# Performance work log

Measured on AMD Instinct MI355X. Metric: run time of the kernel, lower is better.

## Reference

```python
import jax, jax.numpy as jnp
import numpy as np

D_MODEL = 1024
N_HEADS = 16
D_K = D_MODEL // N_HEADS
D_FF = 4096
EPS = 1e-5


def _layernorm(x, g, b):
    mu = jnp.mean(x, axis=-1, keepdims=True)
    var = jnp.var(x, axis=-1, keepdims=True)
    return (x - mu) * jax.lax.rsqrt(var + EPS) * g + b


def setup_inputs() -> dict:
    key = jax.random.key(0)
    ks = jax.random.split(key, 12)
    s = 0.02
    x = jax.random.normal(ks[0], (2, 2048, D_MODEL), dtype=jnp.float32)
    # Linear weights stored [in, out] so y = x @ W + b
    wq = jax.random.normal(ks[1], (D_MODEL, D_MODEL), dtype=jnp.float32) * s
    wk = jax.random.normal(ks[2], (D_MODEL, D_MODEL), dtype=jnp.float32) * s
    wv = jax.random.normal(ks[3], (D_MODEL, D_MODEL), dtype=jnp.float32) * s
    wo = jax.random.normal(ks[4], (D_MODEL, D_MODEL), dtype=jnp.float32) * s
    bq = jnp.zeros((D_MODEL,), jnp.float32)
    bk = jnp.zeros((D_MODEL,), jnp.float32)
    bv = jnp.zeros((D_MODEL,), jnp.float32)
    bo = jnp.zeros((D_MODEL,), jnp.float32)
    ln1_g = jnp.ones((D_MODEL,), jnp.float32)
    ln1_b = jnp.zeros((D_MODEL,), jnp.float32)
    ln2_g = jnp.ones((D_MODEL,), jnp.float32)
    ln2_b = jnp.zeros((D_MODEL,), jnp.float32)
    w1 = jax.random.normal(ks[5], (D_MODEL, D_FF), dtype=jnp.float32) * s
    b1 = jnp.zeros((D_FF,), jnp.float32)
    w2 = jax.random.normal(ks[6], (D_FF, D_MODEL), dtype=jnp.float32) * s
    b2 = jnp.zeros((D_MODEL,), jnp.float32)
    return {"x": x, "wq": wq, "bq": bq, "wk": wk, "bk": bk, "wv": wv, "bv": bv,
            "wo": wo, "bo": bo, "ln1_g": ln1_g, "ln1_b": ln1_b,
            "ln2_g": ln2_g, "ln2_b": ln2_b, "w1": w1, "b1": b1, "w2": w2, "b2": b2}


def reference(x, wq, bq, wk, bk, wv, bv, wo, bo, ln1_g, ln1_b, ln2_g, ln2_b, w1, b1, w2, b2):
    B, S, _ = x.shape
    res = x
    # project and split heads: [B, S, H, Dk]
    q = (x @ wq + bq).reshape(B, S, N_HEADS, D_K)
    k = (x @ wk + bk).reshape(B, S, N_HEADS, D_K)
    v = (x @ wv + bv).reshape(B, S, N_HEADS, D_K)
    # full score matrix [B, H, Sq, Sk] (faithful to unfused original)
    scores = jnp.einsum('bqhd,bkhd->bhqk', q, k) / jnp.sqrt(jnp.float32(D_K))
    weights = jax.nn.softmax(scores, axis=-1)
    attn = jnp.einsum('bhqk,bkhd->bqhd', weights, v).reshape(B, S, D_MODEL)
    x = _layernorm(res + attn @ wo + bo, ln1_g, ln1_b)
    res = x
    h = jax.nn.relu(x @ w1 + b1)
    x = _layernorm(res + h @ w2 + b2, ln2_g, ln2_b)
    return x
```

## Files before the change

### kernel.cpp

```cpp
#include <hip/hip_runtime.h>
#include <hip/hip_bf16.h>
#include <stdint.h>


typedef __hip_bfloat16 bf16;
typedef short bf16x8 __attribute__((ext_vector_type(8)));
typedef float f32x4 __attribute__((ext_vector_type(4)));

#if __has_builtin(__builtin_amdgcn_exp2f)
#define EXP2F(x) __builtin_amdgcn_exp2f(x)
#else
#define EXP2F(x) exp2f(x)
#endif

__device__ __forceinline__ float bf2f_lo(unsigned u) { return __uint_as_float(u << 16); }
__device__ __forceinline__ float bf2f_hi(unsigned u) { return __uint_as_float(u & 0xffff0000u); }
__device__ __forceinline__ ushort f2bf(float f) {
  union { bf16 h; ushort u; } c; c.h = __float2bfloat16(f); return c.u;
}
__device__ __forceinline__ uint pk_bf16(float a, float b) {
  union { __hip_bfloat162 h2; uint u; } c;
  c.h2 = __float22bfloat162_rn(make_float2(a, b));
  return c.u;
}
__device__ __forceinline__ bool is_f32(const uint* probe) { return probe[0] == 0x3F800000u; }
__device__ __forceinline__ float ld_param(const void* p, size_t i, bool f32) {
  return f32 ? ((const float*)p)[i] : __bfloat162float(((const bf16*)p)[i]);
}

__device__ __forceinline__ void barrier_raw() {
  asm volatile("" ::: "memory");
  __builtin_amdgcn_s_barrier();
  asm volatile("" ::: "memory");
}
__device__ __forceinline__ void lgkm0() {
  asm volatile("s_waitcnt lgkmcnt(0)" ::: "memory");
}
__device__ __forceinline__ void glds16(const ushort* g, ushort* l) {
  __builtin_amdgcn_global_load_lds(
      (const __attribute__((address_space(1))) void*)g,
      (__attribute__((address_space(3))) void*)l, 16, 0, 0);
}

#define MFMA16(MH, NH)                                                        \
  do {                                                                        \
    _Pragma("unroll") for (int c_ = 0; c_ < 2; ++c_)                          \
    _Pragma("unroll") for (int fi_ = 0; fi_ < 4; ++fi_)                       \
    _Pragma("unroll") for (int gi_ = 0; gi_ < 2; ++gi_)                       \
      acc[(MH) * 4 + fi_][(NH) * 2 + gi_] =                                   \
          __builtin_amdgcn_mfma_f32_16x16x32_bf16(                            \
              areg[fi_][c_], breg[(NH) * 2 + gi_][c_],                        \
              acc[(MH) * 4 + fi_][(NH) * 2 + gi_], 0, 0, 0);                  \
  } while (0)

__device__ __forceinline__ void gemm256_body(
    const ushort* __restrict__ A, const ushort* __restrict__ BT,
    const void* __restrict__ bias, const void* __restrict__ res,
    void* __restrict__ C, int N_, int K_, int bm, int bn,
    int kb, int ke, int mode, const uint* probe) {
  __shared__ ushort As[2][16384];
  __shared__ ushort Bs[2][16384];

  const int tid = threadIdx.x;
  const int wave = tid >> 6;
  const int lane = tid & 63;
  const int wm = wave >> 2;
  const int wn = wave & 3;
  const int m16 = lane & 15;
  const int quad = lane >> 4;
  const int nt = (ke - kb) >> 6;

  const int srow = lane >> 2;
  const int skc = ((lane & 3) * 8) ^ (((lane >> 5) & 1) << 4);
  const ushort* pA = A + (size_t)(bm * 256 + wave * 16 + srow) * K_ + kb + skc;
  const ushort* pB = BT + (size_t)(bn * 256 + wave * 16 + srow) * K_ + kb + skc;
  const size_t hstep = (size_t)128 * K_;
  ushort* dA = &As[0][0] + wave * 1024;
  ushort* dB = &Bs[0][0] + wave * 1024;

  auto stageA = [&](int b, int half, int t) {
    const ushort* g = pA + (size_t)half * hstep + t * 64;
    ushort* d = dA + b * 16384 + half * 8192;
    glds16(g, d);
    glds16(g + 32, d + 512);
  };
  auto stageB = [&](int b, int half, int t) {
    const ushort* g = pB + (size_t)half * hstep + t * 64;
    ushort* d = dB + b * 16384 + half * 8192;
    glds16(g, d);
    glds16(g + 32, d + 512);
  };

  const int fr_off = m16 * 32 + ((quad * 8) ^ (((m16 >> 3) & 1) << 4));
  const ushort* rA = &As[0][0] + fr_off;
  const ushort* rB = &Bs[0][0] + fr_off;
  auto ldA = [&](int b, int f, int c) {
    return *(const bf16x8*)(rA + b * 16384 +
                            ((f >> 2) * 8 + wm * 4 + (f & 3)) * 1024 + c * 512);
  };
  auto ldB = [&](int b, int g, int c) {
    return *(const bf16x8*)(rB + b * 16384 +
                            ((g >> 1) * 8 + wn * 2 + (g & 1)) * 1024 + c * 512);
  };

  f32x4 acc[8][4];
#pragma unroll
  for (int f = 0; f < 8; ++f)
#pragma unroll
    for (int g = 0; g < 4; ++g) acc[f][g] = (f32x4){0.f, 0.f, 0.f, 0.f};
  bf16x8 areg[4][2], breg[4][2];

  stageA(0, 0, 0); stageB(0, 0, 0); stageA(0, 1, 0); stageB(0, 1, 0);
  if (nt > 1) { stageA(1, 0, 1); stageB(1, 0, 1); }
  asm volatile("s_waitcnt vmcnt(4)" ::: "memory");
  barrier_raw();

  for (int t = 0; t < nt; ++t) {
    const int b = t & 1, bo = b ^ 1;
#pragma unroll
    for (int fi = 0; fi < 4; ++fi) { areg[fi][0] = ldA(b, fi, 0); areg[fi][1] = ldA(b, fi, 1); }
#pragma unroll
    for (int gi = 0; gi < 2; ++gi) { breg[gi][0] = ldB(b, gi, 0); breg[gi][1] = ldB(b, gi, 1); }
    if (t + 1 < nt) stageA(bo, 1, t + 1);
    barrier_raw(); lgkm0();
    __builtin_amdgcn_s_setprio(1); MFMA16(0, 0); __builtin_amdgcn_s_setprio(0);
    barrier_raw();
#pragma unroll
    for (int gi = 2; gi < 4; ++gi) { breg[gi][0] = ldB(b, gi, 0); breg[gi][1] = ldB(b, gi, 1); }
    if (t + 1 < nt) stageB(bo, 1, t + 1);
    barrier_raw(); lgkm0();
    __builtin_amdgcn_s_setprio(1); MFMA16(0, 1); __builtin_amdgcn_s_setprio(0);
    barrier_raw();
#pragma unroll
    for (int fi = 0; fi < 4; ++fi) { areg[fi][0] = ldA(b, fi + 4, 0); areg[fi][1] = ldA(b, fi + 4, 1); }
    if (t + 2 < nt) stageA(b, 0, t + 2);
    barrier_raw(); lgkm0();
    __builtin_amdgcn_s_setprio(1); MFMA16(1, 0); __builtin_amdgcn_s_setprio(0);
    barrier_raw();
    if (t + 2 < nt) stageB(b, 0, t + 2);
    barrier_raw(); lgkm0();
    __builtin_amdgcn_s_setprio(1); MFMA16(1, 1); __builtin_amdgcn_s_setprio(0);
    if (t + 2 < nt) asm volatile("s_waitcnt vmcnt(4)" ::: "memory");
    else            asm volatile("s_waitcnt vmcnt(0)" ::: "memory");
    barrier_raw();
  }

  const bool F32 = is_f32(probe);
#pragma unroll
  for (int g = 0; g < 4; ++g) {
    const int col = bn * 256 + (g >> 1) * 128 + wn * 32 + (g & 1) * 16 + m16;
    const float bv = (mode >= 3) ? 0.f : ld_param(bias, col, F32);
#pragma unroll
    for (int f = 0; f < 8; ++f) {
      const int rowb = bm * 256 + (f >> 2) * 128 + wm * 64 + (f & 3) * 16 + quad * 4;
#pragma unroll
      for (int r = 0; r < 4; ++r) {
        const int row = rowb + r;
        float v = acc[f][g][r] + bv;
        if (mode == 1) v = fmaxf(v, 0.f);
        if (mode == 2) v += __bfloat162float(((const bf16*)res)[(size_t)row * N_ + col]);
        if (mode == 2 || mode == 3) ((float*)C)[(size_t)row * N_ + col] = v;
        else ((bf16*)C)[(size_t)row * N_ + col] = __float2bfloat16(v);
      }
    }
  }
}

__global__ __launch_bounds__(512, 2) void gemm256_qkv(
    const ushort* A, const ushort* BT0, const ushort* BT1, const ushort* BT2,
    const void* b0, const void* b1, const void* b2,
    bf16* C0, bf16* C1, bf16* C2, const uint* probe) {
  const int sel = blockIdx.y >> 2, bn = blockIdx.y & 3;
  const ushort* BT = sel == 0 ? BT0 : (sel == 1 ? BT1 : BT2);
  const void* bb = sel == 0 ? b0 : (sel == 1 ? b1 : b2);
  bf16* C = sel == 0 ? C0 : (sel == 1 ? C1 : C2);
  gemm256_body(A, BT, bb, nullptr, C, 1024, 1024, blockIdx.x, bn, 0, 1024, 0, probe);
}
__global__ __launch_bounds__(512, 2) void gemm256_ffn1(
    const ushort* A, const ushort* BT, const void* bias, bf16* C, const uint* probe) {
  gemm256_body(A, BT, bias, nullptr, C, 4096, 1024,
               blockIdx.x, blockIdx.y, 0, 1024, 1, probe);
}
__global__ __launch_bounds__(512, 2) void gemm256_ffn2_sk4(
    const ushort* A, const ushort* BT,
    bf16* P0, bf16* P1, bf16* P2, bf16* P3, const uint* probe) {
  const int kz = blockIdx.z;
  bf16* C = kz == 0 ? P0 : kz == 1 ? P1 : kz == 2 ? P2 : P3;
  gemm256_body(A, BT, nullptr, nullptr, C, 1024, 4096, blockIdx.x, blockIdx.y,
               kz * 1024, kz * 1024 + 1024, 4, probe);
}

template <bool A_EXT, bool RES_EXT>
__device__ __forceinline__ void gemm_body(
    const void* __restrict__ Av, const ushort* __restrict__ BT,
    const void* __restrict__ bias, const void* __restrict__ res,
    void* __restrict__ C, int N_, int K_, int bm, int bn,
    int kb, int ke, int mode, const uint* probe) {
  __shared__ ushort Asm_[128 * 32];
  __shared__ ushort Bsm_[128 * 32];

  const bool F32 = is_f32(probe);
  const bool AF = A_EXT && F32;

  const int tid = threadIdx.x;
  const int wave = tid >> 6;
  const int lane = tid & 63;
  const int wm = wave & 1, wn = wave >> 1;

  const int r0 = tid >> 2;
  const int c0 = (tid & 3) * 8;
  const int dA0 = r0 * 32 + c0;
  const int dA1 = dA0 + 64 * 32;

  const size_t aRow0 = (size_t)(bm * 128 + r0) * K_;
  const size_t aRow1 = aRow0 + (size_t)64 * K_;
  const ushort* pB0 = BT + (size_t)(bn * 128 + r0) * K_ + c0;
  const ushort* pB1 = pB0 + (size_t)64 * K_;

  auto ld4 = [&](int kk, uint4& A0, uint4& A1, uint4& B0, uint4& B1) {
    if (AF) {
      const float* Af = (const float*)Av;
      const float4 f0 = *(const float4*)(Af + aRow0 + kk + c0);
      const float4 f1 = *(const float4*)(Af + aRow0 + kk + c0 + 4);
      const float4 g0 = *(const float4*)(Af + aRow1 + kk + c0);
      const float4 g1 = *(const float4*)(Af + aRow1 + kk + c0 + 4);
      A0.x = pk_bf16(f0.x, f0.y); A0.y = pk_bf16(f0.z, f0.w);
      A0.z = pk_bf16(f1.x, f1.y); A0.w = pk_bf16(f1.z, f1.w);
      A1.x = pk_bf16(g0.x, g0.y); A1.y = pk_bf16(g0.z, g0.w);
      A1.z = pk_bf16(g1.x, g1.y); A1.w = pk_bf16(g1.z, g1.w);
    } else {
      const ushort* Ab = (const ushort*)Av;
      A0 = *(const uint4*)(Ab + aRow0 + kk + c0);
      A1 = *(const uint4*)(Ab + aRow1 + kk + c0);
    }
    B0 = *(const uint4*)(pB0 + kk);
    B1 = *(const uint4*)(pB1 + kk);
  };

  f32x4 zero = {0.f, 0.f, 0.f, 0.f};
  f32x4 acc[4][4];
#pragma unroll
  for (int i = 0; i < 4; ++i)
#pragma unroll
    for (int j = 0; j < 4; ++j) acc[i][j] = zero;

  const int m16 = lane & 15;
  const int quad = lane >> 4;
  const int koff = quad * 8;

  uint4 a0, a1, b0, b1;
  ld4(kb, a0, a1, b0, b1);

  for (int k0 = kb; k0 < ke; k0 += 32) {
    __syncthreads();
    *(uint4*)&Asm_[dA0] = a0;
    *(uint4*)&Asm_[dA1] = a1;
    *(uint4*)&Bsm_[dA0] = b0;
    *(uint4*)&Bsm_[dA1] = b1;
    __syncthreads();

    if (k0 + 32 < ke) ld4(k0 + 32, a0, a1, b0, b1);

    bf16x8 af[4], bfr[4];
#pragma unroll
    for (int i = 0; i < 4; ++i)
      af[i] = *(const bf16x8*)&Asm_[(wm * 64 + i * 16 + m16) * 32 + koff];
#pragma unroll
    for (int j = 0; j < 4; ++j)
      bfr[j] = *(const bf16x8*)&Bsm_[(wn * 64 + j * 16 + m16) * 32 + koff];
#pragma unroll
    for (int i = 0; i < 4; ++i)
#pragma unroll
      for (int j = 0; j < 4; ++j)
        acc[i][j] = __builtin_amdgcn_mfma_f32_16x16x32_bf16(af[i], bfr[j], acc[i][j], 0, 0, 0);
  }

  const int row0 = bm * 128 + wm * 64;
  const int col0 = bn * 128 + wn * 64;
#pragma unroll
  for (int j = 0; j < 4; ++j) {
    const int col = col0 + j * 16 + m16;
    const float bv = (mode == 3) ? 0.f : ld_param(bias, col, F32);
#pragma unroll
    for (int i = 0; i < 4; ++i) {
#pragma unroll
      for (int r = 0; r < 4; ++r) {
        const int row = row0 + i * 16 + quad * 4 + r;
        float v = acc[i][j][r] + bv;
        if (mode == 1) v = fmaxf(v, 0.f);
        if (mode == 2) v += ld_param(res, (size_t)row * N_ + col, RES_EXT && F32);
        if (mode >= 2) ((float*)C)[(size_t)row * N_ + col] = v;
        else ((bf16*)C)[(size_t)row * N_ + col] = __float2bfloat16(v);
      }
    }
  }
}

__global__ __launch_bounds__(256) void gemm_wo_sk(
    const ushort* A, const ushort* BT, const void* bias, const void* res,
    float* C0, float* C1, const uint* probe) {
  const int kz = blockIdx.z;
  gemm_body<false, true>(A, BT, bias, res, kz ? C1 : C0, 1024, 1024,
                         blockIdx.x, blockIdx.y, kz * 512, kz * 512 + 512,
                         kz ? 3 : 2, probe);
}

__global__ __launch_bounds__(256) void transpose_all(
    const void* W0, const void* W1, const void* W2, const void* W3,
    const void* W4, const void* W5, const void* X6,
    ushort* D0, ushort* D1, ushort* D2, ushort* D3, ushort* D4, ushort* D5,
    ushort* D6, const uint* probe) {
  const int z = blockIdx.z;
  if (z == 6) {
    const bool F32 = is_f32(probe);
    const size_t i =
        ((size_t)(blockIdx.y * 128 + blockIdx.x) * 256 + threadIdx.x) * 4;
    if (F32) {
      const float4 a = *(const float4*)((const float*)X6 + i);
      uint2 o; o.x = pk_bf16(a.x, a.y); o.y = pk_bf16(a.z, a.w);
      *(uint2*)(D6 + i) = o;
    } else {
      *(uint2*)(D6 + i) = *(const uint2*)((const ushort*)X6 + i);
    }
    return;
  }
  if (z < 4 && blockIdx.x >= 32) return;
  int n0, k0, K_, N_;
  const void* W;
  ushort* D;
  if (z < 4) {
    n0 = blockIdx.x * 32; k0 = blockIdx.y * 32; K_ = 1024; N_ = 1024;
    W = z == 0 ? W0 : z == 1 ? W1 : z == 2 ? W2 : W3;
    D = z == 0 ? D0 : z == 1 ? D1 : z == 2 ? D2 : D3;
  } else if (z == 4) {
    n0 = blockIdx.x * 32; k0 = blockIdx.y * 32; K_ = 1024; N_ = 4096; W = W4; D = D4;
  } else {
    n0 = blockIdx.y * 32; k0 = blockIdx.x * 32; K_ = 4096; N_ = 1024; W = W5; D = D5;
  }
  const bool F32 = is_f32(probe);
  __shared__ ushort tile[32][33];
  const int tx = threadIdx.x & 31, ty = threadIdx.x >> 5;
#pragma unroll
  for (int i = 0; i < 32; i += 8) {
    const size_t src = (size_t)(k0 + ty + i) * N_ + n0 + tx;
    tile[ty + i][tx] = F32 ? f2bf(((const float*)W)[src]) : ((const ushort*)W)[src];
  }
  __syncthreads();
#pragma unroll
  for (int i = 0; i < 32; i += 8)
    D[(size_t)(n0 + ty + i) * K_ + k0 + tx] = tile[tx][ty + i];
}

template <bool OUT_EXT>
__global__ __launch_bounds__(256) void ln_kernel(
    const float* __restrict__ X, const float* __restrict__ P,
    const void* __restrict__ g, const void* __restrict__ bta,
    void* __restrict__ out, const uint* probe) {
  const bool F32 = is_f32(probe);
  const int row = blockIdx.x;
  const int tid = threadIdx.x;
  const float4 a = *(const float4*)(X + (size_t)row * 1024 + tid * 4);
  const float4 b = *(const float4*)(P + (size_t)row * 1024 + tid * 4);
  const float xv[4] = {a.x + b.x, a.y + b.y, a.z + b.z, a.w + b.w};
  float s = xv[0] + xv[1] + xv[2] + xv[3];
  float ss = xv[0] * xv[0] + xv[1] * xv[1] + xv[2] * xv[2] + xv[3] * xv[3];
#pragma unroll
  for (int o = 32; o > 0; o >>= 1) { s += __shfl_down(s, o); ss += __shfl_down(ss, o); }
  __shared__ float red[8];
  if ((tid & 63) == 0) { red[tid >> 6] = s; red[4 + (tid >> 6)] = ss; }
  __syncthreads();
  s = red[0] + red[1] + red[2] + red[3];
  ss = red[4] + red[5] + red[6] + red[7];
  const float mu = s * (1.f / 1024.f);
  const float rstd = rsqrtf(ss * (1.f / 1024.f) - mu * mu + 1e-5f);
#pragma unroll
  for (int i = 0; i < 4; ++i) {
    const size_t idx = (size_t)row * 1024 + tid * 4 + i;
    const float y = (xv[i] - mu) * rstd * ld_param(g, tid * 4 + i, F32) +
                    ld_param(bta, tid * 4 + i, F32);
    if (OUT_EXT && F32) ((float*)out)[idx] = y;
    else ((bf16*)out)[idx] = __float2bfloat16(y);
  }
}

template <bool OUT_EXT>
__global__ __launch_bounds__(256) void ln4_kernel(
    const ushort* __restrict__ P0, const ushort* __restrict__ P1,
    const ushort* __restrict__ P2, const ushort* __restrict__ P3,
    const ushort* __restrict__ resX, const void* __restrict__ b2,
    const void* __restrict__ g, const void* __restrict__ bta,
    void* __restrict__ out, const uint* probe) {
  const bool F32 = is_f32(probe);
  const int row = blockIdx.x;
  const int tid = threadIdx.x;
  const size_t base = (size_t)row * 1024 + tid * 4;
  float xv[4];
  {
    const uint2 ur = *(const uint2*)(resX + base);
    xv[0] = bf2f_lo(ur.x) + ld_param(b2, tid * 4 + 0, F32);
    xv[1] = bf2f_hi(ur.x) + ld_param(b2, tid * 4 + 1, F32);
    xv[2] = bf2f_lo(ur.y) + ld_param(b2, tid * 4 + 2, F32);
    xv[3] = bf2f_hi(ur.y) + ld_param(b2, tid * 4 + 3, F32);
  }
  auto addv = [&](const ushort* P) {
    const uint2 u = *(const uint2*)(P + base);
    xv[0] += bf2f_lo(u.x); xv[1] += bf2f_hi(u.x);
    xv[2] += bf2f_lo(u.y); xv[3] += bf2f_hi(u.y);
  };
  addv(P0); addv(P1); addv(P2); addv(P3);
  float s = xv[0] + xv[1] + xv[2] + xv[3];
  float ss = xv[0] * xv[0] + xv[1] * xv[1] + xv[2] * xv[2] + xv[3] * xv[3];
#pragma unroll
  for (int o = 32; o > 0; o >>= 1) { s += __shfl_down(s, o); ss += __shfl_down(ss, o); }
  __shared__ float red[8];
  if ((tid & 63) == 0) { red[tid >> 6] = s; red[4 + (tid >> 6)] = ss; }
  __syncthreads();
  s = red[0] + red[1] + red[2] + red[3];
  ss = red[4] + red[5] + red[6] + red[7];
  const float mu = s * (1.f / 1024.f);
  const float rstd = rsqrtf(ss * (1.f / 1024.f) - mu * mu + 1e-5f);
#pragma unroll
  for (int i = 0; i < 4; ++i) {
    const size_t idx = base + i;
    const float y = (xv[i] - mu) * rstd * ld_param(g, tid * 4 + i, F32) +
                    ld_param(bta, tid * 4 + i, F32);
    if (OUT_EXT && F32) ((float*)out)[idx] = y;
    else ((bf16*)out)[idx] = __float2bfloat16(y);
  }
}

__global__ __launch_bounds__(256) void attn_mfma(
    const ushort* __restrict__ Qm, const ushort* __restrict__ Km,
    const ushort* __restrict__ Vm, ushort* __restrict__ Om) {
  __shared__ ushort Ks[64 * 72];
  __shared__ ushort Vt[64 * 72];
  __shared__ ushort Pw[4][32 * 72];

  const int tid = threadIdx.x;
  const int wave = tid >> 6, lane = tid & 63;
  const int m16 = lane & 15, quad = lane >> 4;
  const int bb = blockIdx.z, h = blockIdx.y;
  const size_t hb = ((size_t)bb * 2048) * 1024 + h * 64;
  const int q0 = blockIdx.x * 128 + wave * 32;

  const float QS = 0.125f * 1.44269504f;
  bf16x8 qf[2][2];
#pragma unroll
  for (int i = 0; i < 2; ++i)
#pragma unroll
    for (int c = 0; c < 2; ++c) {
      const uint4 u = *(const uint4*)(Qm + hb + (size_t)(q0 + 16 * i + m16) * 1024 + c * 32 + quad * 8);
      const uint w[4] = {u.x, u.y, u.z, u.w};
      bf16x8 f;
#pragma unroll
      for (int j = 0; j < 4; ++j) {
        const uint p = pk_bf16(bf2f_lo(w[j]) * QS, bf2f_hi(w[j]) * QS);
        f[2 * j]     = (short)(p & 0xffffu);
        f[2 * j + 1] = (short)(p >> 16);
      }
      qf[i][c] = f;
    }

  f32x4 zero = {0.f, 0.f, 0.f, 0.f};
  f32x4 acc[2][4];
#pragma unroll
  for (int i = 0; i < 2; ++i)
#pragma unroll
    for (int j = 0; j < 4; ++j) acc[i][j] = zero;
  float lp[2][4] = {{0.f, 0.f, 0.f, 0.f}, {0.f, 0.f, 0.f, 0.f}};

  const int skey = tid >> 2;
  const int sd = (tid & 3) * 8;
  const int pp = tid & 31;
  const int dc = tid >> 5;
  const int ka_ = 16 * ((2 * pp) & 3) + ((2 * pp) >> 2);
  const int kb_ = 16 * ((2 * pp + 1) & 3) + ((2 * pp + 1) >> 2);
  const ushort* Kg = Km + hb;
  const ushort* Vg = Vm + hb;

  uint4 kr0, kr1, vr0, vr1;
  kr0 = *(const uint4*)(Kg + (size_t)skey * 1024 + sd);
  kr1 = *(const uint4*)(Kg + (size_t)skey * 1024 + sd + 32);
  vr0 = *(const uint4*)(Vg + (size_t)ka_ * 1024 + dc * 8);
  vr1 = *(const uint4*)(Vg + (size_t)kb_ * 1024 + dc * 8);

  for (int kt = 0; kt < 2048; kt += 64) {
    __syncthreads();
    *(uint4*)&Ks[skey * 72 + sd] = kr0;
    *(uint4*)&Ks[skey * 72 + sd + 32] = kr1;
    {
      const uint va[4] = {vr0.x, vr0.y, vr0.z, vr0.w};
      const uint vb[4] = {vr1.x, vr1.y, vr1.z, vr1.w};
#pragma unroll
      for (int j = 0; j < 8; ++j) {
        const uint lo = (j & 1) ? (va[j >> 1] >> 16) : (va[j >> 1] & 0xffffu);
        const uint hi = (j & 1) ? (vb[j >> 1] & 0xffff0000u) : (vb[j >> 1] << 16);
        *(uint*)&Vt[(dc * 8 + j) * 72 + 2 * pp] = lo | hi;
      }
    }
    __syncthreads();

    if (kt + 64 < 2048) {
      kr0 = *(const uint4*)(Kg + (size_t)(kt + 64 + skey) * 1024 + sd);
      kr1 = *(const uint4*)(Kg + (size_t)(kt + 64 + skey) * 1024 + sd + 32);
      vr0 = *(const uint4*)(Vg + (size_t)(kt + 64 + ka_) * 1024 + dc * 8);
      vr1 = *(const uint4*)(Vg + (size_t)(kt + 64 + kb_) * 1024 + dc * 8);
    }

    f32x4 s[2][4];
#pragma unroll
    for (int i = 0; i < 2; ++i)
#pragma unroll
      for (int jn = 0; jn < 4; ++jn) s[i][jn] = zero;
#pragma unroll
    for (int c = 0; c < 2; ++c) {
      bf16x8 kb4[4];
#pragma unroll
      for (int jn = 0; jn < 4; ++jn)
        kb4[jn] = *(const bf16x8*)&Ks[(jn * 16 + m16) * 72 + c * 32 + quad * 8];
#pragma unroll
      for (int i = 0; i < 2; ++i)
#pragma unroll
        for (int jn = 0; jn < 4; ++jn)
          s[i][jn] = __builtin_amdgcn_mfma_f32_16x16x32_bf16(qf[i][c], kb4[jn], s[i][jn], 0, 0, 0);
    }

#pragma unroll
    for (int i = 0; i < 2; ++i)
#pragma unroll
      for (int r = 0; r < 4; ++r) {
        const float p0 = EXP2F(s[i][0][r]);
        const float p1 = EXP2F(s[i][1][r]);
        const float p2 = EXP2F(s[i][2][r]);
        const float p3 = EXP2F(s[i][3][r]);
        lp[i][r] += (p0 + p1) + (p2 + p3);
        uint2 pk;
        pk.x = pk_bf16(p0, p1);
        pk.y = pk_bf16(p2, p3);
        *(uint2*)&Pw[wave][(16 * i + quad * 4 + r) * 72 + m16 * 4] = pk;
      }
    asm volatile("s_waitcnt lgkmcnt(0)" ::: "memory");

#pragma unroll
    for (int c = 0; c < 2; ++c) {
      bf16x8 pa[2], vb4[4];
#pragma unroll
      for (int i = 0; i < 2; ++i)
        pa[i] = *(const bf16x8*)&Pw[wave][(16 * i + m16) * 72 + c * 32 + quad * 8];
#pragma unroll
      for (int jd = 0; jd < 4; ++jd)
        vb4[jd] = *(const bf16x8*)&Vt[(jd * 16 + m16) * 72 + c * 32 + quad * 8];
#pragma unroll
      for (int i = 0; i < 2; ++i)
#pragma unroll
        for (int jd = 0; jd < 4; ++jd)
          acc[i][jd] = __builtin_amdgcn_mfma_f32_16x16x32_bf16(pa[i], vb4[jd], acc[i][jd], 0, 0, 0);
    }
  }

#pragma unroll
  for (int i = 0; i < 2; ++i)
#pragma unroll
    for (int r = 0; r < 4; ++r) {
      float l = lp[i][r];
      l += __shfl_xor(l, 1); l += __shfl_xor(l, 2);
      l += __shfl_xor(l, 4); l += __shfl_xor(l, 8);
      const float inv = 1.f / l;
      const size_t rowoff = hb + (size_t)(q0 + 16 * i + quad * 4 + r) * 1024;
#pragma unroll
      for (int jd = 0; jd < 4; ++jd)
        Om[rowoff + jd * 16 + m16] = f2bf(acc[i][jd][r] * inv);
    }
}

extern "C" void kernel_launch(void* const* d_in, const int* in_sizes, int n_in,
                              void* d_out, int out_size, void* d_ws, size_t ws_size,
                              hipStream_t stream) {
  const void* x   = d_in[0];
  const void* wq  = d_in[1];
  const void* bq  = d_in[2];
  const void* wk  = d_in[3];
  const void* bk  = d_in[4];
  const void* wv  = d_in[5];
  const void* bv  = d_in[6];
  const void* wo  = d_in[7];
  const void* bo  = d_in[8];
  const uint* probe = (const uint*)d_in[9];
  const void* ln1g = d_in[9];
  const void* ln1b = d_in[10];
  const void* ln2g = d_in[11];
  const void* ln2b = d_in[12];
  const void* w1  = d_in[13];
  const void* b1  = d_in[14];
  const void* w2  = d_in[15];
  const void* b2  = d_in[16];

  char* ws = (char*)d_ws;
  const size_t MB = 1ull << 20;
  ushort* wqT = (ushort*)(ws + 0 * MB);
  ushort* wkT = (ushort*)(ws + 2 * MB);
  ushort* wvT = (ushort*)(ws + 4 * MB);
  ushort* woT = (ushort*)(ws + 6 * MB);
  ushort* w1T = (ushort*)(ws + 8 * MB);
  ushort* w2T = (ushort*)(ws + 16 * MB);
  ushort* Qb  = (ushort*)(ws + 24 * MB);
  ushort* Kb  = (ushort*)(ws + 32 * MB);
  ushort* Vb  = (ushort*)(ws + 40 * MB);
  ushort* Xb  = (ushort*)(ws + 64 * MB);
  ushort* AO  = (ushort*)(ws + 72 * MB);
  float*  T1  = (float*)(ws + 24 * MB);
  float*  P1w = (float*)(ws + 40 * MB);
  ushort* X1  = (ushort*)(ws + 56 * MB);
  ushort* Hb  = (ushort*)(ws + 24 * MB);
  ushort* P2a = (ushort*)(ws + 0 * MB);
  ushort* P2b = (ushort*)(ws + 8 * MB);
  ushort* P2c = (ushort*)(ws + 64 * MB);
  ushort* P2d = (ushort*)(ws + 72 * MB);

  const dim3 blk(256);
  const dim3 blk512(512);
  transpose_all<<<dim3(128, 32, 7), blk, 0, stream>>>(
      wq, wk, wv, wo, w1, w2, x, wqT, wkT, wvT, woT, w1T, w2T, Xb, probe);

  gemm256_qkv<<<dim3(16, 12), blk512, 0, stream>>>(
      Xb, wqT, wkT, wvT, bq, bk, bv, (bf16*)Qb, (bf16*)Kb, (bf16*)Vb, probe);
  attn_mfma<<<dim3(16, 16, 2), blk, 0, stream>>>(Qb, Kb, Vb, AO);
  gemm_wo_sk<<<dim3(32, 8, 2), blk, 0, stream>>>(AO, woT, bo, x, T1, P1w, probe);
  ln_kernel<false><<<dim3(4096), blk, 0, stream>>>(T1, P1w, ln1g, ln1b, X1, probe);
  gemm256_ffn1<<<dim3(16, 16), blk512, 0, stream>>>(X1, w1T, b1, (bf16*)Hb, probe);
  gemm256_ffn2_sk4<<<dim3(16, 4, 4), blk512, 0, stream>>>(
      Hb, w2T, (bf16*)P2a, (bf16*)P2b, (bf16*)P2c, (bf16*)P2d, probe);
  ln4_kernel<true><<<dim3(4096), blk, 0, stream>>>(
      P2a, P2b, P2c, P2d, X1, b2, ln2g, ln2b, d_out, probe);
}
```

Before: 355.6 us.

## Restructure attention kernel with async K loads, swizzled LDS, smaller tiles

The attention kernel now loads K tiles straight into double-buffered LDS with global-to-LDS loads, which removes the register staging step. LDS layouts for K, V-transpose and P switch from padded rows to XOR-swizzled layouts to avoid bank conflicts. Each wave now handles 16 query rows instead of 32, giving 1024 blocks on a 1D grid remapped so neighbouring blocks spread across heads, and wave priority is raised around the MFMA sections. Smaller tiles mean each K/V tile loaded into LDS is reused across fewer query rows, but occupancy should be higher.

Result: no change. 354.7 us (-0.3%).

```diff
diff --git a/kernel.cpp b/kernel.cpp
--- a/kernel.cpp
+++ b/kernel.cpp
@@ -429,65 +429,72 @@
   }
 }
 
-__global__ __launch_bounds__(256) void attn_mfma(
+__global__ __launch_bounds__(256, 4) void attn_mfma(
     const ushort* __restrict__ Qm, const ushort* __restrict__ Km,
     const ushort* __restrict__ Vm, ushort* __restrict__ Om) {
-  __shared__ ushort Ks[64 * 72];
-  __shared__ ushort Vt[64 * 72];
-  __shared__ ushort Pw[4][32 * 72];
+  __shared__ ushort Ks[2][4096];
+  __shared__ ushort Vt[4096];
+  __shared__ ushort Pw[4][1024];
 
   const int tid = threadIdx.x;
   const int wave = tid >> 6, lane = tid & 63;
   const int m16 = lane & 15, quad = lane >> 4;
-  const int bb = blockIdx.z, h = blockIdx.y;
-  const size_t hb = ((size_t)bb * 2048) * 1024 + h * 64;
-  const int q0 = blockIdx.x * 128 + wave * 32;
+
+  const int g = blockIdx.x;
+  const int slot = g >> 3;
+  const int bh = (g & 7) * 4 + (slot >> 5);
+  const int qt = slot & 31;
+  const int bb = bh >> 4, h = bh & 15;
+  const size_t hb = ((size_t)bb * 2048) * 1024 + (size_t)h * 64;
+  const int q0 = qt * 64 + wave * 16;
 
   const float QS = 0.125f * 1.44269504f;
-  bf16x8 qf[2][2];
-#pragma unroll
-  for (int i = 0; i < 2; ++i)
-#pragma unroll
-    for (int c = 0; c < 2; ++c) {
-      const uint4 u = *(const uint4*)(Qm + hb + (size_t)(q0 + 16 * i + m16) * 1024 + c * 32 + quad * 8);
-      const uint w[4] = {u.x, u.y, u.z, u.w};
-      bf16x8 f;
-#pragma unroll
-      for (int j = 0; j < 4; ++j) {
-        const uint p = pk_bf16(bf2f_lo(w[j]) * QS, bf2f_hi(w[j]) * QS);
-        f[2 * j]     = (short)(p & 0xffffu);
-        f[2 * j + 1] = (short)(p >> 16);
-      }
-      qf[i][c] = f;
-    }
+  const int swz = (m16 >> 3) << 4;
+  const int rdo = m16 * 32 + ((quad * 8) ^ swz);
+
+  bf16x8 qf[2];
+#pragma unroll
+  for (int c = 0; c < 2; ++c) {
+    const uint4 u = *(const uint4*)(Qm + hb + (size_t)(q0 + m16) * 1024 + c * 32 + quad * 8);
+    const uint w[4] = {u.x, u.y, u.z, u.w};
+    bf16x8 f;
+#pragma unroll
+    for (int j = 0; j < 4; ++j) {
+      const uint p = pk_bf16(bf2f_lo(w[j]) * QS, bf2f_hi(w[j]) * QS);
+      f[2 * j]     = (short)(p & 0xffffu);
+      f[2 * j + 1] = (short)(p >> 16);
+    }
+    qf[c] = f;
+  }
 
   f32x4 zero = {0.f, 0.f, 0.f, 0.f};
-  f32x4 acc[2][4];
-#pragma unroll
-  for (int i = 0; i < 2; ++i)
-#pragma unroll
-    for (int j = 0; j < 4; ++j) acc[i][j] = zero;
-  float lp[2][4] = {{0.f, 0.f, 0.f, 0.f}, {0.f, 0.f, 0.f, 0.f}};
-
-  const int skey = tid >> 2;
-  const int sd = (tid & 3) * 8;
+  f32x4 acc[4];
+#pragma unroll
+  for (int jd = 0; jd < 4; ++jd) acc[jd] = zero;
+  float lp[4] = {0.f, 0.f, 0.f, 0.f};
+
+  const int srow = lane >> 2;
+  const int skc = ((lane & 3) * 8) ^ ((lane >> 5) << 4);
+  const ushort* pK = Km + hb + (size_t)(wave * 16 + srow) * 1024 + skc;
+  ushort* dK = &Ks[0][0] + wave * 1024;
+
   const int pp = tid & 31;
   const int dc = tid >> 5;
   const int ka_ = 16 * ((2 * pp) & 3) + ((2 * pp) >> 2);
   const int kb_ = 16 * ((2 * pp + 1) & 3) + ((2 * pp + 1) >> 2);
-  const ushort* Kg = Km + hb;
   const ushort* Vg = Vm + hb;
-
-  uint4 kr0, kr1, vr0, vr1;
-  kr0 = *(const uint4*)(Kg + (size_t)skey * 1024 + sd);
-  kr1 = *(const uint4*)(Kg + (size_t)skey * 1024 + sd + 32);
-  vr0 = *(const uint4*)(Vg + (size_t)ka_ * 1024 + dc * 8);
-  vr1 = *(const uint4*)(Vg + (size_t)kb_ * 1024 + dc * 8);
+  const int vtb = (dc >> 1) * 1024 + (pp >> 4) * 512 + (dc & 1) * 256 +
+                  ((2 * (pp & 15)) ^ ((dc & 1) << 4));
+
+  glds16(pK, dK);
+  glds16(pK + 32, dK + 512);
+  uint4 vr0 = *(const uint4*)(Vg + (size_t)ka_ * 1024 + dc * 8);
+  uint4 vr1 = *(const uint4*)(Vg + (size_t)kb_ * 1024 + dc * 8);
+  asm volatile("s_waitcnt vmcnt(2)" ::: "memory");
 
   for (int kt = 0; kt < 2048; kt += 64) {
+    const int b = (kt >> 6) & 1;
     __syncthreads();
-    *(uint4*)&Ks[skey * 72 + sd] = kr0;
-    *(uint4*)&Ks[skey * 72 + sd + 32] = kr1;
     {
       const uint va[4] = {vr0.x, vr0.y, vr0.z, vr0.w};
       const uint vb[4] = {vr1.x, vr1.y, vr1.z, vr1.w};
@@ -495,82 +502,80 @@
       for (int j = 0; j < 8; ++j) {
         const uint lo = (j & 1) ? (va[j >> 1] >> 16) : (va[j >> 1] & 0xffffu);
         const uint hi = (j & 1) ? (vb[j >> 1] & 0xffff0000u) : (vb[j >> 1] << 16);
-        *(uint*)&Vt[(dc * 8 + j) * 72 + 2 * pp] = lo | hi;
+        *(uint*)&Vt[vtb + j * 32] = lo | hi;
       }
     }
+    if (kt + 64 < 2048) {
+      const ushort* gk = pK + (size_t)(kt + 64) * 1024;
+      ushort* d = dK + (b ^ 1) * 4096;
+      glds16(gk, d);
+      glds16(gk + 32, d + 512);
+    }
     __syncthreads();
-
     if (kt + 64 < 2048) {
-      kr0 = *(const uint4*)(Kg + (size_t)(kt + 64 + skey) * 1024 + sd);
-      kr1 = *(const uint4*)(Kg + (size_t)(kt + 64 + skey) * 1024 + sd + 32);
       vr0 = *(const uint4*)(Vg + (size_t)(kt + 64 + ka_) * 1024 + dc * 8);
       vr1 = *(const uint4*)(Vg + (size_t)(kt + 64 + kb_) * 1024 + dc * 8);
     }
 
-    f32x4 s[2][4];
-#pragma unroll
-    for (int i = 0; i < 2; ++i)
-#pragma unroll
-      for (int jn = 0; jn < 4; ++jn) s[i][jn] = zero;
+    f32x4 s[4];
+#pragma unroll
+    for (int jn = 0; jn < 4; ++jn) s[jn] = zero;
+    __builtin_amdgcn_s_setprio(1);
 #pragma unroll
     for (int c = 0; c < 2; ++c) {
       bf16x8 kb4[4];
 #pragma unroll
       for (int jn = 0; jn < 4; ++jn)
-        kb4[jn] = *(const bf16x8*)&Ks[(jn * 16 + m16) * 72 + c * 32 + quad * 8];
-#pragma unroll
-      for (int i = 0; i < 2; ++i)
-#pragma unroll
-        for (int jn = 0; jn < 4; ++jn)
-          s[i][jn] = __builtin_amdgcn_mfma_f32_16x16x32_bf16(qf[i][c], kb4[jn], s[i][jn], 0, 0, 0);
-    }
-
-#pragma unroll
-    for (int i = 0; i < 2; ++i)
-#pragma unroll
-      for (int r = 0; r < 4; ++r) {
-        const float p0 = EXP2F(s[i][0][r]);
-        const float p1 = EXP2F(s[i][1][r]);
-        const float p2 = EXP2F(s[i][2][r]);
-        const float p3 = EXP2F(s[i][3][r]);
-        lp[i][r] += (p0 + p1) + (p2 + p3);
-        uint2 pk;
-        pk.x = pk_bf16(p0, p1);
-        pk.y = pk_bf16(p2, p3);
-        *(uint2*)&Pw[wave][(16 * i + quad * 4 + r) * 72 + m16 * 4] = pk;
-      }
-    asm volatile("s_waitcnt lgkmcnt(0)" ::: "memory");
-
+        kb4[jn] = *(const bf16x8*)&Ks[b][jn * 1024 + c * 512 + rdo];
+#pragma unroll
+      for (int jn = 0; jn < 4; ++jn)
+        s[jn] = __builtin_amdgcn_mfma_f32_16x16x32_bf16(qf[c], kb4[jn], s[jn], 0, 0, 0);
+    }
+    __builtin_amdgcn_s_setprio(0);
+
+#pragma unroll
+    for (int r = 0; r < 4; ++r) {
+      const float p0 = EXP2F(s[0][r]);
+      const float p1 = EXP2F(s[1][r]);
+      const float p2 = EXP2F(s[2][r]);
+      const float p3 = EXP2F(s[3][r]);
+      lp[r] += (p0 + p1) + (p2 + p3);
+      uint2 pk2;
+      pk2.x = pk_bf16(p0, p1);
+      pk2.y = pk_bf16(p2, p3);
+      const int row = quad * 4 + r;
+      *(uint2*)&Pw[wave][(m16 >> 3) * 512 + row * 32 +
+                         (((m16 & 7) * 4) ^ ((row >> 3) << 4))] = pk2;
+    }
+    lgkm0();
+
+    __builtin_amdgcn_s_setprio(1);
 #pragma unroll
     for (int c = 0; c < 2; ++c) {
-      bf16x8 pa[2], vb4[4];
-#pragma unroll
-      for (int i = 0; i < 2; ++i)
-        pa[i] = *(const bf16x8*)&Pw[wave][(16 * i + m16) * 72 + c * 32 + quad * 8];
+      bf16x8 vb4[4];
+      const bf16x8 pa = *(const bf16x8*)&Pw[wave][c * 512 + rdo];
 #pragma unroll
       for (int jd = 0; jd < 4; ++jd)
-        vb4[jd] = *(const bf16x8*)&Vt[(jd * 16 + m16) * 72 + c * 32 + quad * 8];
-#pragma unroll
-      for (int i = 0; i < 2; ++i)
-#pragma unroll
-        for (int jd = 0; jd < 4; ++jd)
-          acc[i][jd] = __builtin_amdgcn_mfma_f32_16x16x32_bf16(pa[i], vb4[jd], acc[i][jd], 0, 0, 0);
-    }
-  }
-
-#pragma unroll
-  for (int i = 0; i < 2; ++i)
-#pragma unroll
-    for (int r = 0; r < 4; ++r) {
-      float l = lp[i][r];
-      l += __shfl_xor(l, 1); l += __shfl_xor(l, 2);
-      l += __shfl_xor(l, 4); l += __shfl_xor(l, 8);
-      const float inv = 1.f / l;
-      const size_t rowoff = hb + (size_t)(q0 + 16 * i + quad * 4 + r) * 1024;
+        vb4[jd] = *(const bf16x8*)&Vt[jd * 1024 + c * 512 + rdo];
 #pragma unroll
       for (int jd = 0; jd < 4; ++jd)
-        Om[rowoff + jd * 16 + m16] = f2bf(acc[i][jd][r] * inv);
-    }
+        acc[jd] = __builtin_amdgcn_mfma_f32_16x16x32_bf16(pa, vb4[jd], acc[jd], 0, 0, 0);
+    }
+    __builtin_amdgcn_s_setprio(0);
+    asm volatile("s_waitcnt vmcnt(2)" ::: "memory");
+  }
+
+#pragma unroll
+  for (int r = 0; r < 4; ++r) {
+    float l = lp[r];
+    l += __shfl_xor(l, 1); l += __shfl_xor(l, 2);
+    l += __shfl_xor(l, 4); l += __shfl_xor(l, 8);
+    const float inv = 1.f / l;
+    const size_t rowoff = hb + (size_t)(q0 + quad * 4 + r) * 1024;
+#pragma unroll
+    for (int jd = 0; jd < 4; ++jd)
+      Om[rowoff + jd * 16 + m16] = f2bf(acc[jd][r] * inv);
+  }
 }
 
 extern "C" void kernel_launch(void* const* d_in, const int* in_sizes, int n_in,
@@ -624,7 +629,7 @@
 
   gemm256_qkv<<<dim3(16, 12), blk512, 0, stream>>>(
       Xb, wqT, wkT, wvT, bq, bk, bv, (bf16*)Qb, (bf16*)Kb, (bf16*)Vb, probe);
-  attn_mfma<<<dim3(16, 16, 2), blk, 0, stream>>>(Qb, Kb, Vb, AO);
+  attn_mfma<<<dim3(1024), blk, 0, stream>>>(Qb, Kb, Vb, AO);
   gemm_wo_sk<<<dim3(32, 8, 2), blk, 0, stream>>>(AO, woT, bo, x, T1, P1w, probe);
   ln_kernel<false><<<dim3(4096), blk, 0, stream>>>(T1, P1w, ln1g, ln1b, X1, probe);
   gemm256_ffn1<<<dim3(16, 16), blk512, 0, stream>>>(X1, w1T, b1, (bf16*)Hb, probe);
```
